# Kernel tuning notes

Hardware: AMD Instinct MI355X
Metric: run time of the kernel (lower is better)

The kernel has to match this reference:

```python
import jax, jax.numpy as jnp
import numpy as np

D_MODEL = 1024
N_HEADS = 16
HEAD_DIM = D_MODEL // N_HEADS


def setup_inputs() -> dict:
    key = jax.random.key(0)
    k1, k2, k3, k4, k5 = jax.random.split(key, 5)
    s = 1.0 / np.sqrt(D_MODEL)
    return {
        "x": jax.random.normal(k1, (2, 2048, D_MODEL), dtype=jnp.float32),
        "w_qkv": jax.random.normal(k2, (D_MODEL, 3 * D_MODEL), dtype=jnp.float32) * s,
        "b_qkv": jax.random.normal(k3, (3 * D_MODEL,), dtype=jnp.float32) * 0.02,
        "w_proj": jax.random.normal(k4, (D_MODEL, D_MODEL), dtype=jnp.float32) * s,
        "b_proj": jax.random.normal(k5, (D_MODEL,), dtype=jnp.float32) * 0.02,
    }


def reference(x, w_qkv, b_qkv, w_proj, b_proj):
    B, S, D = x.shape
    H, Hd = N_HEADS, HEAD_DIM
    qkv = x @ w_qkv + b_qkv                       # [B,S,3D]
    q, k, v = jnp.split(qkv, 3, axis=-1)
    # split heads -> [B,H,S,Hd]
    q = q.reshape(B, S, H, Hd).transpose(0, 2, 1, 3)
    k = k.reshape(B, S, H, Hd).transpose(0, 2, 1, 3)
    v = v.reshape(B, S, H, Hd).transpose(0, 2, 1, 3)
    scale = 1.0 / jnp.sqrt(jnp.asarray(Hd, dtype=x.dtype))
    scores = jnp.einsum("bhqd,bhkd->bhqk", q, k) * scale  # [B,H,S,S]
    causal = jnp.tril(jnp.ones((S, S), dtype=bool))
    scores = jnp.where(causal, scores, jnp.asarray(-jnp.inf, dtype=scores.dtype))
    attn = jax.nn.softmax(scores, axis=-1)
    out = jnp.einsum("bhqk,bhkd->bhqd", attn, v)  # [B,H,S,Hd]
    out = out.transpose(0, 2, 1, 3).reshape(B, S, D)
    return out @ w_proj + b_proj
```

## Files before the change

kernel.cpp:

```cpp
#include <hip/hip_runtime.h>


typedef float f32x4 __attribute__((ext_vector_type(4)));
typedef float f32x16 __attribute__((ext_vector_type(16)));
typedef short bf16x8 __attribute__((ext_vector_type(8)));

#if __has_builtin(__builtin_amdgcn_exp2f)
#define EXP2(x) __builtin_amdgcn_exp2f(x)
#else
#define EXP2(x) exp2f(x)
#endif

__device__ __forceinline__ unsigned short f2bf(float f) {
  union { float f; unsigned u; } v; v.f = f;
  unsigned u = v.u + 0x7fffu + ((v.u >> 16) & 1u);
  return (unsigned short)(u >> 16);
}

__device__ __forceinline__ void async_load16(const void* g, void* lds) {
  __builtin_amdgcn_global_load_lds(
      (const __attribute__((address_space(1))) void*)g,
      (__attribute__((address_space(3))) void*)lds, 16, 0, 0);
}

__global__ __launch_bounds__(256) void prep_kernel(
    const float* __restrict__ x, const float* __restrict__ w_qkv,
    const float* __restrict__ w_proj, unsigned short* __restrict__ Xb,
    unsigned short* __restrict__ WTq, unsigned short* __restrict__ WTp)
{
  const int bid = blockIdx.x;
  const int tid = threadIdx.x;
  if (bid < 4096) {
    const int i = (bid * 256 + tid) * 4;
    float4 f = *(const float4*)(x + i);
    ushort4 o;
    o.x = f2bf(f.x); o.y = f2bf(f.y); o.z = f2bf(f.z); o.w = f2bf(f.w);
    *(ushort4*)(Xb + i) = o;
  } else {
    __shared__ float tile[32][33];
    const float* in; unsigned short* out; int N, bx, by;
    if (bid < 7168) { const int b2 = bid - 4096; in = w_qkv;  out = WTq; N = 3072; bx = b2 % 96; by = b2 / 96; }
    else            { const int b3 = bid - 7168; in = w_proj; out = WTp; N = 1024; bx = b3 & 31; by = b3 >> 5; }
    const int tx = tid & 31, ty = tid >> 5;
    const int n0 = bx * 32, k0 = by * 32;
#pragma unroll
    for (int i = ty; i < 32; i += 8)
      tile[i][tx] = in[(size_t)(k0 + i) * N + (n0 + tx)];
    __syncthreads();
#pragma unroll
    for (int i = ty; i < 32; i += 8)
      out[(size_t)(n0 + i) * 1024 + (k0 + tx)] = f2bf(tile[tx][i]);
  }
}

template <int MI, int NI>
__device__ __forceinline__ void gemm_mainloop(
    const unsigned short* __restrict__ A,
    const unsigned short* __restrict__ BT,
    int K, int mBlk, int nBlk,
    unsigned short* As, unsigned short* Bs,
    f32x4 (&acc)[MI][NI], int lane, int wave)
{
  const int l16 = lane & 15, quad = lane >> 4;
  const int mW = (wave >> 1) * MI * 16;
  const int nW = (wave & 1) * NI * 16;
  constexpr int AROWS = 2 * MI * 16;
  constexpr int BROWS = 2 * NI * 16;
  constexpr int AINST = AROWS / 64;
  constexpr int BINST = BROWS / 64;
  const int rl = lane >> 2;
  const int cl = (lane & 3) * 8;

  for (int k0 = 0; k0 < K; k0 += 32) {
    __syncthreads();
#pragma unroll
    for (int t = 0; t < AINST; ++t) {
      const int rbase = wave * (AROWS / 4) + t * 16;
      async_load16(A + (size_t)(mBlk + rbase + rl) * K + k0 + cl, &As[rbase * 32]);
    }
#pragma unroll
    for (int t = 0; t < BINST; ++t) {
      const int rbase = wave * (BROWS / 4) + t * 16;
      async_load16(BT + (size_t)(nBlk + rbase + rl) * K + k0 + cl, &Bs[rbase * 32]);
    }
    __syncthreads();

    bf16x8 af[MI], bf[NI];
#pragma unroll
    for (int i = 0; i < MI; ++i)
      af[i] = *(const bf16x8*)&As[(mW + i * 16 + l16) * 32 + quad * 8];
#pragma unroll
    for (int j = 0; j < NI; ++j)
      bf[j] = *(const bf16x8*)&Bs[(nW + j * 16 + l16) * 32 + quad * 8];
#pragma unroll
    for (int i = 0; i < MI; ++i)
#pragma unroll
      for (int j = 0; j < NI; ++j)
        acc[i][j] = __builtin_amdgcn_mfma_f32_16x16x32_bf16(af[i], bf[j], acc[i][j], 0, 0, 0);
  }
}

__global__ __launch_bounds__(512, 2) void qkv_gemm_kernel(
    const unsigned short* __restrict__ A,
    const unsigned short* __restrict__ WT,
    const float* __restrict__ bias,
    unsigned short* __restrict__ QKV)
{
  __shared__ __align__(16) unsigned short Al[2][2][256][32];
  __shared__ __align__(16) unsigned short Bl[2][2][256][32];
  const int lane = threadIdx.x & 63;
  const int wave = threadIdx.x >> 6;
  const int l16 = lane & 15, quad = lane >> 4;
  const int wm = wave >> 2, wn = wave & 3;

  const int bid = blockIdx.x;
  const int xcd = bid & 7, rb = bid >> 3;
  const int bx = (xcd & 3) * 4 + (rb & 3);
  const int by = (xcd >> 2) * 6 + (rb >> 2);
  const int mBlk = bx * 256, nBlk = by * 256;

  const int srow = wave * 32 + (lane >> 2);
  const int scol = lane & 3;

  auto stage = [&](const unsigned short* __restrict__ G, int gRow0,
                   unsigned short (*L)[32], int kOff) {
#pragma unroll
    for (int i = 0; i < 2; ++i) {
      const int row = srow + i * 16;
      const int c = scol ^ ((row >> 1) & 3);
      async_load16(G + (size_t)(gRow0 + row) * 1024 + kOff + c * 8,
                   &L[wave * 32 + i * 16][0]);
    }
  };

  auto rdA = [&](int buf, int kh, int mi) -> bf16x8 {
    const int r = wm * 128 + mi * 16 + l16;
    return *(const bf16x8*)&Al[buf][kh][r][(quad ^ ((r >> 1) & 3)) * 8];
  };
  auto rdB = [&](int buf, int kh, int n) -> bf16x8 {
    const int r = wn * 64 + n * 16 + l16;
    return *(const bf16x8*)&Bl[buf][kh][r][(quad ^ ((r >> 1) & 3)) * 8];
  };

  f32x4 acc[8][4];
  const f32x4 z4 = {0.f, 0.f, 0.f, 0.f};
#pragma unroll
  for (int i = 0; i < 8; ++i)
#pragma unroll
    for (int j = 0; j < 4; ++j) acc[i][j] = z4;

  stage(A, mBlk, Al[0][0], 0);
  stage(WT, nBlk, Bl[0][0], 0);
  stage(A, mBlk, Al[0][1], 32);
  stage(WT, nBlk, Bl[0][1], 32);
  asm volatile("s_waitcnt vmcnt(4)\n\ts_barrier" ::: "memory");

  for (int t = 0; t < 16; ++t) {
    const int cur = t & 1, nxt = cur ^ 1;
    const int tn = (t + 1 < 16) ? t + 1 : 15;
    const int kO = tn * 64;
    bf16x8 bfr[4], afr[8];

    stage(A, mBlk, Al[nxt][0], kO);
    stage(WT, nBlk, Bl[nxt][0], kO);
#pragma unroll
    for (int n = 0; n < 4; ++n) bfr[n] = rdB(cur, 0, n);
#pragma unroll
    for (int i = 0; i < 8; ++i) afr[i] = rdA(cur, 0, i);
    __builtin_amdgcn_s_setprio(1);
#pragma unroll
    for (int i = 0; i < 8; ++i)
#pragma unroll
      for (int n = 0; n < 4; ++n)
        acc[i][n] = __builtin_amdgcn_mfma_f32_16x16x32_bf16(afr[i], bfr[n], acc[i][n], 0, 0, 0);
    __builtin_amdgcn_s_setprio(0);
    asm volatile("s_waitcnt vmcnt(4)\n\ts_barrier" ::: "memory");

    stage(A, mBlk, Al[nxt][1], kO + 32);
    stage(WT, nBlk, Bl[nxt][1], kO + 32);
#pragma unroll
    for (int n = 0; n < 4; ++n) bfr[n] = rdB(cur, 1, n);
#pragma unroll
    for (int i = 0; i < 8; ++i) afr[i] = rdA(cur, 1, i);
    __builtin_amdgcn_s_setprio(1);
#pragma unroll
    for (int i = 0; i < 8; ++i)
#pragma unroll
      for (int n = 0; n < 4; ++n)
        acc[i][n] = __builtin_amdgcn_mfma_f32_16x16x32_bf16(afr[i], bfr[n], acc[i][n], 0, 0, 0);
    __builtin_amdgcn_s_setprio(0);
    asm volatile("s_waitcnt vmcnt(4)\n\ts_barrier" ::: "memory");
  }
  asm volatile("s_waitcnt vmcnt(0)" ::: "memory");

  const int m0 = mBlk + wm * 128;
  const int n0 = nBlk + wn * 64;
  const int whichW = n0 >> 10;
  const int bb = m0 >> 11;
  const int sBase = (m0 & 2047);
  const size_t planeE = (size_t)2 * 16 * 2048 * 64;

  if (whichW == 2) {
    unsigned short* Vb = QKV + 2 * planeE;
#pragma unroll
    for (int j = 0; j < 4; ++j) {
      const int rem = (n0 & 1023) + j * 16 + l16;
      const int hh = rem >> 6, hd = rem & 63;
      const float bv = bias[n0 + j * 16 + l16];
      unsigned short* col = Vb + (((size_t)bb * 16 + hh) * 64 + hd) * 2048;
#pragma unroll
      for (int i = 0; i < 8; ++i) {
        unsigned short pk[4];
#pragma unroll
        for (int r = 0; r < 4; ++r) pk[r] = f2bf(acc[i][j][r] + bv);
        *(ushort4*)&col[sBase + i * 16 + quad * 4] = *(ushort4*)pk;
      }
    }
  } else {
    const float scale = (whichW == 0) ? 0.18033688011112042f : 1.0f;
#pragma unroll
    for (int j = 0; j < 4; ++j) {
      const int n = n0 + j * 16 + l16;
      const float bv = bias[n];
      const int rem = n & 1023;
      const int hh = rem >> 6, hd = rem & 63;
      unsigned short* pl = QKV + (size_t)whichW * planeE +
                           (((size_t)bb * 16 + hh) * 2048) * 64 + hd;
#pragma unroll
      for (int r = 0; r < 4; ++r) {
        const int s = sBase + (quad * 4 + r);
#pragma unroll
        for (int i = 0; i < 8; ++i)
          pl[(size_t)(s + i * 16) * 64] = f2bf((acc[i][j][r] + bv) * scale);
      }
    }
  }
}

__global__ __launch_bounds__(256, 2) void attn_kernel(
    const unsigned short* __restrict__ QKV,
    unsigned short* __restrict__ AO)
{
  __shared__ __align__(16) unsigned short Ks[3 * 64 * 64];
  __shared__ __align__(16) unsigned short Vs[3 * 64 * 64];
  const int lane = threadIdx.x & 63;
  const int wave = threadIdx.x >> 6;
  const int l31 = lane & 31;
  const int hi  = lane >> 5;

  const int lin  = blockIdx.x;
  const int xcd  = lin & 7;
  const int slot = lin >> 3;
  const int col  = xcd * 4 + (slot >> 4);
  const int b = col >> 4, h = col & 15;
  const int qg = (slot < 32) ? (slot & 15) : (15 - (slot & 15));
  const int qw = qg * 128 + wave * 32;

  const size_t planeE = (size_t)2 * 16 * 2048 * 64;
  const size_t bhS = ((size_t)b * 16 + h) * (size_t)(2048 * 64);
  const unsigned short* Q   = QKV + bhS;
  const unsigned short* Kg  = QKV + planeE + bhS;
  const unsigned short* VTg = QKV + 2 * planeE + bhS;

  bf16x8 qf_[4];
#pragma unroll
  for (int t = 0; t < 4; ++t)
    qf_[t] = *(const bf16x8*)(Q + (size_t)(qw + l31) * 64 + t * 16 + hi * 8);

  bf16x8 onesf;
#pragma unroll
  for (int i = 0; i < 8; ++i) onesf[i] = (short)0x3F80;

  f32x16 O[2], Osum;
#pragma unroll
  for (int r = 0; r < 16; ++r) { O[0][r] = 0.f; O[1][r] = 0.f; Osum[r] = 0.f; }

  const int tbase = (wave & 1) * 4;
  const bool doV = wave >= 2;

  auto stage = [&](int tileIdx, int bufIdx) {
    const int kt = tileIdx * 64;
    unsigned short* Kb = Ks + bufIdx * 4096;
    unsigned short* Vb = Vs + bufIdx * 4096;
#pragma unroll
    for (int i = 0; i < 4; ++i) {
      const int t = tbase + i;
      const int s = t * 64 + lane;
      const int row = s >> 3;
      const int c = (s & 7) ^ (row & 7);
      if (doV)
        async_load16(VTg + (size_t)row * 2048 + kt + c * 8, Vb + t * 512);
      else
        async_load16(Kg + (size_t)(kt + row) * 64 + c * 8, Kb + t * 512);
    }
  };

  const int nt = qg * 2 + 2;
  stage(0, 0);
  stage(1, 1);
  for (int ti = 0; ti < nt; ++ti) {
    asm volatile("s_waitcnt vmcnt(4)\n\ts_barrier" ::: "memory");
    const int tn = (ti + 2 < nt) ? ti + 2 : nt - 1;
    stage(tn, (ti + 2) % 3);
    const int kt = ti * 64;
    const unsigned short* Kb = Ks + (ti % 3) * 4096;
    const unsigned short* Vb = Vs + (ti % 3) * 4096;

    if (kt <= qw + 31) {
      const bool dmask = (kt + 63 > qw);
#pragma unroll
      for (int kg = 0; kg < 2; ++kg) {
        const int krow = kg * 32 + l31;
        const int ks7 = krow & 7;
        bf16x8 ka[4];
#pragma unroll
        for (int t = 0; t < 4; ++t)
          ka[t] = *(const bf16x8*)&Kb[(krow * 8 + ((t * 2 + hi) ^ ks7)) * 8];

        f32x16 sc;
#pragma unroll
        for (int r = 0; r < 16; ++r) sc[r] = 0.f;
        __builtin_amdgcn_s_setprio(1);
#pragma unroll
        for (int t = 0; t < 4; ++t)
          sc = __builtin_amdgcn_mfma_f32_32x32x16_bf16(ka[t], qf_[t], sc, 0, 0, 0);
        __builtin_amdgcn_s_setprio(0);

        float p[16];
#pragma unroll
        for (int r = 0; r < 16; ++r) {
          float v = sc[r];
          if (dmask) {
            const int key = kt + kg * 32 + (r & 3) + 8 * (r >> 2) + 4 * hi;
            if (key > qw + l31) v = -INFINITY;
          }
          p[r] = EXP2(v);
        }
        unsigned c8[8];
#pragma unroll
        for (int i = 0; i < 8; ++i)
          asm("v_cvt_pk_bf16_f32 %0, %1, %2"
              : "=v"(c8[i]) : "v"(p[2 * i]), "v"(p[2 * i + 1]));

#pragma unroll
        for (int half = 0; half < 2; ++half) {
          unsigned a0 = c8[4 * half + 0], a1 = c8[4 * half + 1];
          unsigned a2 = c8[4 * half + 2], a3 = c8[4 * half + 3];
          asm("v_permlane32_swap_b32 %0, %1" : "+v"(a0), "+v"(a2));
          asm("v_permlane32_swap_b32 %0, %1" : "+v"(a1), "+v"(a3));
          union { unsigned u[4]; bf16x8 v; } pa;
          pa.u[0] = a0; pa.u[1] = a1; pa.u[2] = a2; pa.u[3] = a3;
          const int kc = kg * 2 + half;

          __builtin_amdgcn_s_setprio(1);
          Osum = __builtin_amdgcn_mfma_f32_32x32x16_bf16(pa.v, onesf, Osum, 0, 0, 0);
#pragma unroll
          for (int g = 0; g < 2; ++g) {
            const int vrow = g * 32 + l31;
            bf16x8 vb = *(const bf16x8*)&Vb[(vrow * 8 + ((kc * 2 + hi) ^ (vrow & 7))) * 8];
            O[g] = __builtin_amdgcn_mfma_f32_32x32x16_bf16(pa.v, vb, O[g], 0, 0, 0);
          }
          __builtin_amdgcn_s_setprio(0);
        }
      }
    }
  }

  unsigned short* base = AO + ((size_t)b * 2048 + qw) * 1024 + h * 64 + l31;
#pragma unroll
  for (int r = 0; r < 16; ++r) {
    const float inv = 1.0f / Osum[r];
    const int row = (r & 3) + 8 * (r >> 2) + 4 * hi;
#pragma unroll
    for (int g = 0; g < 2; ++g)
      base[(size_t)row * 1024 + g * 32] = f2bf(O[g][r] * inv);
  }
}

__global__ __launch_bounds__(256) void proj_gemm_kernel(
    const unsigned short* __restrict__ A,
    const unsigned short* __restrict__ WT,
    const float* __restrict__ bias,
    float* __restrict__ out)
{
  __shared__ unsigned short As[64 * 32];
  __shared__ unsigned short Bs[128 * 32];
  const int lane = threadIdx.x & 63;
  const int wave = threadIdx.x >> 6;
  const int l16 = lane & 15, quad = lane >> 4;

  f32x4 acc[2][4];
  const f32x4 z4 = {0.f, 0.f, 0.f, 0.f};
#pragma unroll
  for (int i = 0; i < 2; ++i)
#pragma unroll
    for (int j = 0; j < 4; ++j) acc[i][j] = z4;

  gemm_mainloop<2, 4>(A, WT, 1024, blockIdx.x * 64, blockIdx.y * 128,
                      As, Bs, acc, lane, wave);

  const int m0 = blockIdx.x * 64 + (wave >> 1) * 32;
  const int n0 = blockIdx.y * 128 + (wave & 1) * 64;
#pragma unroll
  for (int i = 0; i < 2; ++i) {
#pragma unroll
    for (int j = 0; j < 4; ++j) {
      const int n = n0 + j * 16 + l16;
      const float bv = bias[n];
#pragma unroll
      for (int r = 0; r < 4; ++r) {
        const int m = m0 + i * 16 + quad * 4 + r;
        out[(size_t)m * 1024 + n] = acc[i][j][r] + bv;
      }
    }
  }
}

extern "C" void kernel_launch(void* const* d_in, const int* in_sizes, int n_in,
                              void* d_out, int out_size, void* d_ws, size_t ws_size,
                              hipStream_t stream) {
  const float* x      = (const float*)d_in[0];
  const float* w_qkv  = (const float*)d_in[1];
  const float* b_qkv  = (const float*)d_in[2];
  const float* w_proj = (const float*)d_in[3];
  const float* b_proj = (const float*)d_in[4];
  float* out = (float*)d_out;

  unsigned short* Xb  = (unsigned short*)d_ws;
  unsigned short* WTq = Xb + (size_t)4096 * 1024;
  unsigned short* WTp = WTq + (size_t)3072 * 1024;
  unsigned short* QKV = WTp + (size_t)1024 * 1024;
  unsigned short* AO  = QKV + (size_t)3 * 4096 * 1024;

  prep_kernel<<<8192, 256, 0, stream>>>(x, w_qkv, w_proj, Xb, WTq, WTp);
  qkv_gemm_kernel<<<192, 512, 0, stream>>>(Xb, WTq, b_qkv, QKV);
  attn_kernel<<<512, 256, 0, stream>>>(QKV, AO);
  proj_gemm_kernel<<<dim3(64, 8), 256, 0, stream>>>(AO, WTp, b_proj, out);
}
```

Before: 195.8 us.

## Fuse prep, QKV GEMM, attention and projection into one cooperative persistent kernel

Replaces the four separate launches with a single cooperative kernel of 256 blocks × 512 threads. The kernel runs each stage as a phase separated by grid-wide syncs and reuses one shared-memory buffer across phases. The attention phase pairs a short and a long causal query group in each block so work stays balanced. The projection phase is retiled to 128×128 blocks so it fits the fixed grid. The aim is to remove kernel launch gaps and tail effects, at the cost of grid.sync overhead and fewer, larger blocks for the memory-bound prep phase.

New measurement: 452.2 us. +130.9%, slower.

```diff
diff --git a/kernel.cpp b/kernel.cpp
--- a/kernel.cpp
+++ b/kernel.cpp
@@ -1,4 +1,7 @@
 #include <hip/hip_runtime.h>
+#include <hip/hip_cooperative_groups.h>
+
+namespace cg = cooperative_groups;
 
 
 typedef float f32x4 __attribute__((ext_vector_type(4)));
@@ -23,394 +26,370 @@
       (__attribute__((address_space(3))) void*)lds, 16, 0, 0);
 }
 
-__global__ __launch_bounds__(256) void prep_kernel(
+__global__ __launch_bounds__(512, 2) void fused_kernel(
     const float* __restrict__ x, const float* __restrict__ w_qkv,
-    const float* __restrict__ w_proj, unsigned short* __restrict__ Xb,
-    unsigned short* __restrict__ WTq, unsigned short* __restrict__ WTp)
+    const float* __restrict__ b_qkv, const float* __restrict__ w_proj,
+    const float* __restrict__ b_proj, float* __restrict__ out,
+    unsigned short* __restrict__ Xb, unsigned short* __restrict__ WTq,
+    unsigned short* __restrict__ WTp, unsigned short* __restrict__ QKV,
+    unsigned short* __restrict__ AO)
 {
+  __shared__ __align__(16) unsigned char smem[131072];
+  cg::grid_group grid = cg::this_grid();
   const int bid = blockIdx.x;
   const int tid = threadIdx.x;
-  if (bid < 4096) {
-    const int i = (bid * 256 + tid) * 4;
-    float4 f = *(const float4*)(x + i);
-    ushort4 o;
-    o.x = f2bf(f.x); o.y = f2bf(f.y); o.z = f2bf(f.z); o.w = f2bf(f.w);
-    *(ushort4*)(Xb + i) = o;
-  } else {
-    __shared__ float tile[32][33];
-    const float* in; unsigned short* out; int N, bx, by;
-    if (bid < 7168) { const int b2 = bid - 4096; in = w_qkv;  out = WTq; N = 3072; bx = b2 % 96; by = b2 / 96; }
-    else            { const int b3 = bid - 7168; in = w_proj; out = WTp; N = 1024; bx = b3 & 31; by = b3 >> 5; }
-    const int tx = tid & 31, ty = tid >> 5;
-    const int n0 = bx * 32, k0 = by * 32;
-#pragma unroll
-    for (int i = ty; i < 32; i += 8)
-      tile[i][tx] = in[(size_t)(k0 + i) * N + (n0 + tx)];
-    __syncthreads();
-#pragma unroll
-    for (int i = ty; i < 32; i += 8)
-      out[(size_t)(n0 + i) * 1024 + (k0 + tx)] = f2bf(tile[tx][i]);
+  const int lane = tid & 63;
+  const size_t planeE = (size_t)2 * 16 * 2048 * 64;
+
+  {
+    const int sub = tid >> 8, t256 = tid & 255;
+    float* tf = (float*)smem;
+#pragma unroll 1
+    for (int it = 0; it < 16; ++it) {
+      const int unit = bid * 32 + it * 2 + sub;
+      if (unit < 4096) {
+        const int i = (unit * 256 + t256) * 4;
+        float4 f = *(const float4*)(x + i);
+        ushort4 o;
+        o.x = f2bf(f.x); o.y = f2bf(f.y); o.z = f2bf(f.z); o.w = f2bf(f.w);
+        *(ushort4*)(Xb + i) = o;
+      } else {
+        const float* in; unsigned short* op; int N, bx2, by2;
+        if (unit < 7168) { const int b2 = unit - 4096; in = w_qkv;  op = WTq; N = 3072; bx2 = b2 % 96; by2 = b2 / 96; }
+        else             { const int b3 = unit - 7168; in = w_proj; op = WTp; N = 1024; bx2 = b3 & 31; by2 = b3 >> 5; }
+        const int tx = t256 & 31, ty = t256 >> 5;
+        const int n0 = bx2 * 32, k0 = by2 * 32;
+#pragma unroll
+        for (int i2 = ty; i2 < 32; i2 += 8)
+          tf[(sub * 32 + i2) * 33 + tx] = in[(size_t)(k0 + i2) * N + n0 + tx];
+        __syncthreads();
+#pragma unroll
+        for (int i2 = ty; i2 < 32; i2 += 8)
+          op[(size_t)(n0 + i2) * 1024 + k0 + tx] = f2bf(tf[(sub * 32 + tx) * 33 + i2]);
+        __syncthreads();
+      }
+    }
   }
-}
-
-template <int MI, int NI>
-__device__ __forceinline__ void gemm_mainloop(
-    const unsigned short* __restrict__ A,
-    const unsigned short* __restrict__ BT,
-    int K, int mBlk, int nBlk,
-    unsigned short* As, unsigned short* Bs,
-    f32x4 (&acc)[MI][NI], int lane, int wave)
-{
-  const int l16 = lane & 15, quad = lane >> 4;
-  const int mW = (wave >> 1) * MI * 16;
-  const int nW = (wave & 1) * NI * 16;
-  constexpr int AROWS = 2 * MI * 16;
-  constexpr int BROWS = 2 * NI * 16;
-  constexpr int AINST = AROWS / 64;
-  constexpr int BINST = BROWS / 64;
-  const int rl = lane >> 2;
-  const int cl = (lane & 3) * 8;
-
-  for (int k0 = 0; k0 < K; k0 += 32) {
-    __syncthreads();
-#pragma unroll
-    for (int t = 0; t < AINST; ++t) {
-      const int rbase = wave * (AROWS / 4) + t * 16;
-      async_load16(A + (size_t)(mBlk + rbase + rl) * K + k0 + cl, &As[rbase * 32]);
-    }
-#pragma unroll
-    for (int t = 0; t < BINST; ++t) {
-      const int rbase = wave * (BROWS / 4) + t * 16;
-      async_load16(BT + (size_t)(nBlk + rbase + rl) * K + k0 + cl, &Bs[rbase * 32]);
-    }
-    __syncthreads();
-
-    bf16x8 af[MI], bf[NI];
-#pragma unroll
-    for (int i = 0; i < MI; ++i)
-      af[i] = *(const bf16x8*)&As[(mW + i * 16 + l16) * 32 + quad * 8];
-#pragma unroll
-    for (int j = 0; j < NI; ++j)
-      bf[j] = *(const bf16x8*)&Bs[(nW + j * 16 + l16) * 32 + quad * 8];
-#pragma unroll
-    for (int i = 0; i < MI; ++i)
-#pragma unroll
-      for (int j = 0; j < NI; ++j)
-        acc[i][j] = __builtin_amdgcn_mfma_f32_16x16x32_bf16(af[i], bf[j], acc[i][j], 0, 0, 0);
+  __threadfence();
+  grid.sync();
+
+  if (bid < 192) {
+    unsigned short* AlB = (unsigned short*)smem;
+    unsigned short* BlB = AlB + 32768;
+    const int wave = tid >> 6;
+    const int l16 = lane & 15, quad = lane >> 4;
+    const int wm = wave >> 2, wn = wave & 3;
+    const int xcd = bid & 7, rb = bid >> 3;
+    const int bx = (xcd & 3) * 4 + (rb & 3);
+    const int by = (xcd >> 2) * 6 + (rb >> 2);
+    const int mBlk = bx * 256, nBlk = by * 256;
+    const int srow = wave * 32 + (lane >> 2);
+    const int scol = lane & 3;
+
+    auto stageQ = [&](const unsigned short* __restrict__ G, int gRow0,
+                      unsigned short* L, int kOff) {
+#pragma unroll
+      for (int i = 0; i < 2; ++i) {
+        const int row = srow + i * 16;
+        const int c = scol ^ ((row >> 1) & 3);
+        async_load16(G + (size_t)(gRow0 + row) * 1024 + kOff + c * 8,
+                     L + (wave * 32 + i * 16) * 32);
+      }
+    };
+    auto rdA = [&](int buf, int kh, int mi) -> bf16x8 {
+      const int r = wm * 128 + mi * 16 + l16;
+      return *(const bf16x8*)&AlB[(buf * 2 + kh) * 8192 + r * 32 + (quad ^ ((r >> 1) & 3)) * 8];
+    };
+    auto rdB = [&](int buf, int kh, int n) -> bf16x8 {
+      const int r = wn * 64 + n * 16 + l16;
+      return *(const bf16x8*)&BlB[(buf * 2 + kh) * 8192 + r * 32 + (quad ^ ((r >> 1) & 3)) * 8];
+    };
+
+    f32x4 acc[8][4];
+    const f32x4 z4 = {0.f, 0.f, 0.f, 0.f};
+#pragma unroll
+    for (int i = 0; i < 8; ++i)
+#pragma unroll
+      for (int j = 0; j < 4; ++j) acc[i][j] = z4;
+
+    stageQ(Xb, mBlk, AlB, 0);
+    stageQ(WTq, nBlk, BlB, 0);
+    stageQ(Xb, mBlk, AlB + 8192, 32);
+    stageQ(WTq, nBlk, BlB + 8192, 32);
+    asm volatile("s_waitcnt vmcnt(4)\n\ts_barrier" ::: "memory");
+
+    for (int t = 0; t < 16; ++t) {
+      const int cur = t & 1, nxt = cur ^ 1;
+      const int tn = (t + 1 < 16) ? t + 1 : 15;
+      const int kO = tn * 64;
+      bf16x8 bfr[4], afr[8];
+
+      stageQ(Xb, mBlk, AlB + (nxt * 2 + 0) * 8192, kO);
+      stageQ(WTq, nBlk, BlB + (nxt * 2 + 0) * 8192, kO);
+#pragma unroll
+      for (int n = 0; n < 4; ++n) bfr[n] = rdB(cur, 0, n);
+#pragma unroll
+      for (int i = 0; i < 8; ++i) afr[i] = rdA(cur, 0, i);
+      __builtin_amdgcn_s_setprio(1);
+#pragma unroll
+      for (int i = 0; i < 8; ++i)
+#pragma unroll
+        for (int n = 0; n < 4; ++n)
+          acc[i][n] = __builtin_amdgcn_mfma_f32_16x16x32_bf16(afr[i], bfr[n], acc[i][n], 0, 0, 0);
+      __builtin_amdgcn_s_setprio(0);
+      asm volatile("s_waitcnt vmcnt(4)\n\ts_barrier" ::: "memory");
+
+      stageQ(Xb, mBlk, AlB + (nxt * 2 + 1) * 8192, kO + 32);
+      stageQ(WTq, nBlk, BlB + (nxt * 2 + 1) * 8192, kO + 32);
+#pragma unroll
+      for (int n = 0; n < 4; ++n) bfr[n] = rdB(cur, 1, n);
+#pragma unroll
+      for (int i = 0; i < 8; ++i) afr[i] = rdA(cur, 1, i);
+      __builtin_amdgcn_s_setprio(1);
+#pragma unroll
+      for (int i = 0; i < 8; ++i)
+#pragma unroll
+        for (int n = 0; n < 4; ++n)
+          acc[i][n] = __builtin_amdgcn_mfma_f32_16x16x32_bf16(afr[i], bfr[n], acc[i][n], 0, 0, 0);
+      __builtin_amdgcn_s_setprio(0);
+      asm volatile("s_waitcnt vmcnt(4)\n\ts_barrier" ::: "memory");
+    }
+    asm volatile("s_waitcnt vmcnt(0)" ::: "memory");
+
+    const int m0 = mBlk + wm * 128;
+    const int n0 = nBlk + wn * 64;
+    const int whichW = n0 >> 10;
+    const int bb = m0 >> 11;
+    const int sBase = (m0 & 2047);
+
+    if (whichW == 2) {
+      unsigned short* Vb = QKV + 2 * planeE;
+#pragma unroll
+      for (int j = 0; j < 4; ++j) {
+        const int rem = (n0 & 1023) + j * 16 + l16;
+        const int hh = rem >> 6, hd = rem & 63;
+        const float bv = b_qkv[n0 + j * 16 + l16];
+        unsigned short* colp = Vb + (((size_t)bb * 16 + hh) * 64 + hd) * 2048;
+#pragma unroll
+        for (int i = 0; i < 8; ++i) {
+          unsigned short pk[4];
+#pragma unroll
+          for (int r = 0; r < 4; ++r) pk[r] = f2bf(acc[i][j][r] + bv);
+          *(ushort4*)&colp[sBase + i * 16 + quad * 4] = *(ushort4*)pk;
+        }
+      }
+    } else {
+      const float scale = (whichW == 0) ? 0.18033688011112042f : 1.0f;
+#pragma unroll
+      for (int j = 0; j < 4; ++j) {
+        const int n = n0 + j * 16 + l16;
+        const float bv = b_qkv[n];
+        const int rem = n & 1023;
+        const int hh = rem >> 6, hd = rem & 63;
+        unsigned short* pl = QKV + (size_t)whichW * planeE +
+                             (((size_t)bb * 16 + hh) * 2048) * 64 + hd;
+#pragma unroll
+        for (int r = 0; r < 4; ++r) {
+          const int s = sBase + (quad * 4 + r);
+#pragma unroll
+          for (int i = 0; i < 8; ++i)
+            pl[(size_t)(s + i * 16) * 64] = f2bf((acc[i][j][r] + bv) * scale);
+        }
+      }
+    }
   }
-}
-
-__global__ __launch_bounds__(512, 2) void qkv_gemm_kernel(
-    const unsigned short* __restrict__ A,
-    const unsigned short* __restrict__ WT,
-    const float* __restrict__ bias,
-    unsigned short* __restrict__ QKV)
-{
-  __shared__ __align__(16) unsigned short Al[2][2][256][32];
-  __shared__ __align__(16) unsigned short Bl[2][2][256][32];
-  const int lane = threadIdx.x & 63;
-  const int wave = threadIdx.x >> 6;
-  const int l16 = lane & 15, quad = lane >> 4;
-  const int wm = wave >> 2, wn = wave & 3;
-
-  const int bid = blockIdx.x;
-  const int xcd = bid & 7, rb = bid >> 3;
-  const int bx = (xcd & 3) * 4 + (rb & 3);
-  const int by = (xcd >> 2) * 6 + (rb >> 2);
-  const int mBlk = bx * 256, nBlk = by * 256;
-
-  const int srow = wave * 32 + (lane >> 2);
-  const int scol = lane & 3;
-
-  auto stage = [&](const unsigned short* __restrict__ G, int gRow0,
-                   unsigned short (*L)[32], int kOff) {
-#pragma unroll
-    for (int i = 0; i < 2; ++i) {
-      const int row = srow + i * 16;
-      const int c = scol ^ ((row >> 1) & 3);
-      async_load16(G + (size_t)(gRow0 + row) * 1024 + kOff + c * 8,
-                   &L[wave * 32 + i * 16][0]);
-    }
-  };
-
-  auto rdA = [&](int buf, int kh, int mi) -> bf16x8 {
-    const int r = wm * 128 + mi * 16 + l16;
-    return *(const bf16x8*)&Al[buf][kh][r][(quad ^ ((r >> 1) & 3)) * 8];
-  };
-  auto rdB = [&](int buf, int kh, int n) -> bf16x8 {
-    const int r = wn * 64 + n * 16 + l16;
-    return *(const bf16x8*)&Bl[buf][kh][r][(quad ^ ((r >> 1) & 3)) * 8];
-  };
-
-  f32x4 acc[8][4];
-  const f32x4 z4 = {0.f, 0.f, 0.f, 0.f};
-#pragma unroll
-  for (int i = 0; i < 8; ++i)
-#pragma unroll
-    for (int j = 0; j < 4; ++j) acc[i][j] = z4;
-
-  stage(A, mBlk, Al[0][0], 0);
-  stage(WT, nBlk, Bl[0][0], 0);
-  stage(A, mBlk, Al[0][1], 32);
-  stage(WT, nBlk, Bl[0][1], 32);
-  asm volatile("s_waitcnt vmcnt(4)\n\ts_barrier" ::: "memory");
-
-  for (int t = 0; t < 16; ++t) {
-    const int cur = t & 1, nxt = cur ^ 1;
-    const int tn = (t + 1 < 16) ? t + 1 : 15;
-    const int kO = tn * 64;
-    bf16x8 bfr[4], afr[8];
-
-    stage(A, mBlk, Al[nxt][0], kO);
-    stage(WT, nBlk, Bl[nxt][0], kO);
-#pragma unroll
-    for (int n = 0; n < 4; ++n) bfr[n] = rdB(cur, 0, n);
-#pragma unroll
-    for (int i = 0; i < 8; ++i) afr[i] = rdA(cur, 0, i);
-    __builtin_amdgcn_s_setprio(1);
-#pragma unroll
-    for (int i = 0; i < 8; ++i)
-#pragma unroll
-      for (int n = 0; n < 4; ++n)
-        acc[i][n] = __builtin_amdgcn_mfma_f32_16x16x32_bf16(afr[i], bfr[n], acc[i][n], 0, 0, 0);
-    __builtin_amdgcn_s_setprio(0);
-    asm volatile("s_waitcnt vmcnt(4)\n\ts_barrier" ::: "memory");
-
-    stage(A, mBlk, Al[nxt][1], kO + 32);
-    stage(WT, nBlk, Bl[nxt][1], kO + 32);
-#pragma unroll
-    for (int n = 0; n < 4; ++n) bfr[n] = rdB(cur, 1, n);
-#pragma unroll
-    for (int i = 0; i < 8; ++i) afr[i] = rdA(cur, 1, i);
-    __builtin_amdgcn_s_setprio(1);
-#pragma unroll
-    for (int i = 0; i < 8; ++i)
-#pragma unroll
-      for (int n = 0; n < 4; ++n)
-        acc[i][n] = __builtin_amdgcn_mfma_f32_16x16x32_bf16(afr[i], bfr[n], acc[i][n], 0, 0, 0);
-    __builtin_amdgcn_s_setprio(0);
-    asm volatile("s_waitcnt vmcnt(4)\n\ts_barrier" ::: "memory");
+  __threadfence();
+  grid.sync();
+
+  {
+    unsigned short* Ksu = (unsigned short*)smem;
+    unsigned short* Vsu = Ksu + 12288;
+    const int wave = tid >> 6;
+    const int sub = tid >> 8;
+    const int wave4 = wave & 3;
+    const int l31 = lane & 31, hi = lane >> 5;
+
+    const int xcd = bid & 7, w = bid >> 3;
+    const int col = xcd * 4 + (w >> 3);
+    const int b = col >> 4, h = col & 15;
+    const int p = w & 7;
+    const int qg = sub ? (15 - p) : p;
+    const int qw = qg * 128 + wave4 * 32;
+
+    const size_t bhS = ((size_t)b * 16 + h) * (size_t)(2048 * 64);
+    const unsigned short* Q   = QKV + bhS;
+    const unsigned short* Kg  = QKV + planeE + bhS;
+    const unsigned short* VTg = QKV + 2 * planeE + bhS;
+
+    bf16x8 qf_[4];
+#pragma unroll
+    for (int t = 0; t < 4; ++t)
+      qf_[t] = *(const bf16x8*)(Q + (size_t)(qw + l31) * 64 + t * 16 + hi * 8);
+
+    bf16x8 onesf;
+#pragma unroll
+    for (int i = 0; i < 8; ++i) onesf[i] = (short)0x3F80;
+
+    f32x16 O[2], Osum;
+#pragma unroll
+    for (int r = 0; r < 16; ++r) { O[0][r] = 0.f; O[1][r] = 0.f; Osum[r] = 0.f; }
+
+    const int tbase = (wave4 & 1) * 4;
+    const bool doV = (wave4 >= 2);
+    const bool doStage = (sub == 0);
+
+    auto stage = [&](int tileIdx, int bufIdx) {
+      if (!doStage) return;
+      const int kt = tileIdx * 64;
+      unsigned short* Kb = Ksu + bufIdx * 4096;
+      unsigned short* Vb = Vsu + bufIdx * 4096;
+#pragma unroll
+      for (int i = 0; i < 4; ++i) {
+        const int t = tbase + i;
+        const int s = t * 64 + lane;
+        const int row = s >> 3;
+        const int c = (s & 7) ^ (row & 7);
+        if (doV)
+          async_load16(VTg + (size_t)row * 2048 + kt + c * 8, Vb + t * 512);
+        else
+          async_load16(Kg + (size_t)(kt + row) * 64 + c * 8, Kb + t * 512);
+      }
+    };
+
+    stage(0, 0);
+    stage(1, 1);
+    for (int ti = 0; ti < 32; ++ti) {
+      asm volatile("s_waitcnt vmcnt(4)\n\ts_barrier" ::: "memory");
+      const int tn = (ti + 2 < 32) ? ti + 2 : 31;
+      stage(tn, (ti + 2) % 3);
+      const int kt = ti * 64;
+      const unsigned short* Kb = Ksu + (ti % 3) * 4096;
+      const unsigned short* Vb = Vsu + (ti % 3) * 4096;
+
+      if (kt <= qw + 31) {
+        const bool dmask = (kt + 63 > qw);
+#pragma unroll
+        for (int kg = 0; kg < 2; ++kg) {
+          const int krow = kg * 32 + l31;
+          const int ks7 = krow & 7;
+          bf16x8 ka[4];
+#pragma unroll
+          for (int t = 0; t < 4; ++t)
+            ka[t] = *(const bf16x8*)&Kb[(krow * 8 + ((t * 2 + hi) ^ ks7)) * 8];
+
+          f32x16 sc;
+#pragma unroll
+          for (int r = 0; r < 16; ++r) sc[r] = 0.f;
+          __builtin_amdgcn_s_setprio(1);
+#pragma unroll
+          for (int t = 0; t < 4; ++t)
+            sc = __builtin_amdgcn_mfma_f32_32x32x16_bf16(ka[t], qf_[t], sc, 0, 0, 0);
+          __builtin_amdgcn_s_setprio(0);
+
+          float pp[16];
+#pragma unroll
+          for (int r = 0; r < 16; ++r) {
+            float v = sc[r];
+            if (dmask) {
+              const int key = kt + kg * 32 + (r & 3) + 8 * (r >> 2) + 4 * hi;
+              if (key > qw + l31) v = -INFINITY;
+            }
+            pp[r] = EXP2(v);
+          }
+          unsigned c8[8];
+#pragma unroll
+          for (int i = 0; i < 8; ++i)
+            asm("v_cvt_pk_bf16_f32 %0, %1, %2"
+                : "=v"(c8[i]) : "v"(pp[2 * i]), "v"(pp[2 * i + 1]));
+
+#pragma unroll
+          for (int half = 0; half < 2; ++half) {
+            unsigned a0 = c8[4 * half + 0], a1 = c8[4 * half + 1];
+            unsigned a2 = c8[4 * half + 2], a3 = c8[4 * half + 3];
+            asm("v_permlane32_swap_b32 %0, %1" : "+v"(a0), "+v"(a2));
+            asm("v_permlane32_swap_b32 %0, %1" : "+v"(a1), "+v"(a3));
+            union { unsigned u[4]; bf16x8 v; } pa;
+            pa.u[0] = a0; pa.u[1] = a1; pa.u[2] = a2; pa.u[3] = a3;
+            const int kc = kg * 2 + half;
+
+            __builtin_amdgcn_s_setprio(1);
+            Osum = __builtin_amdgcn_mfma_f32_32x32x16_bf16(pa.v, onesf, Osum, 0, 0, 0);
+#pragma unroll
+            for (int g = 0; g < 2; ++g) {
+              const int vrow = g * 32 + l31;
+              bf16x8 vb = *(const bf16x8*)&Vb[(vrow * 8 + ((kc * 2 + hi) ^ (vrow & 7))) * 8];
+              O[g] = __builtin_amdgcn_mfma_f32_32x32x16_bf16(pa.v, vb, O[g], 0, 0, 0);
+            }
+            __builtin_amdgcn_s_setprio(0);
+          }
+        }
+      }
+    }
+    asm volatile("s_waitcnt vmcnt(0)" ::: "memory");
+
+    unsigned short* base = AO + ((size_t)b * 2048 + qw) * 1024 + h * 64 + l31;
+#pragma unroll
+    for (int r = 0; r < 16; ++r) {
+      const float inv = 1.0f / Osum[r];
+      const int row = (r & 3) + 8 * (r >> 2) + 4 * hi;
+#pragma unroll
+      for (int g = 0; g < 2; ++g)
+        base[(size_t)row * 1024 + g * 32] = f2bf(O[g][r] * inv);
+    }
   }
-  asm volatile("s_waitcnt vmcnt(0)" ::: "memory");
-
-  const int m0 = mBlk + wm * 128;
-  const int n0 = nBlk + wn * 64;
-  const int whichW = n0 >> 10;
-  const int bb = m0 >> 11;
-  const int sBase = (m0 & 2047);
-  const size_t planeE = (size_t)2 * 16 * 2048 * 64;
-
-  if (whichW == 2) {
-    unsigned short* Vb = QKV + 2 * planeE;
-#pragma unroll
-    for (int j = 0; j < 4; ++j) {
-      const int rem = (n0 & 1023) + j * 16 + l16;
-      const int hh = rem >> 6, hd = rem & 63;
-      const float bv = bias[n0 + j * 16 + l16];
-      unsigned short* col = Vb + (((size_t)bb * 16 + hh) * 64 + hd) * 2048;
-#pragma unroll
-      for (int i = 0; i < 8; ++i) {
-        unsigned short pk[4];
-#pragma unroll
-        for (int r = 0; r < 4; ++r) pk[r] = f2bf(acc[i][j][r] + bv);
-        *(ushort4*)&col[sBase + i * 16 + quad * 4] = *(ushort4*)pk;
-      }
-    }
-  } else {
-    const float scale = (whichW == 0) ? 0.18033688011112042f : 1.0f;
-#pragma unroll
-    for (int j = 0; j < 4; ++j) {
-      const int n = n0 + j * 16 + l16;
-      const float bv = bias[n];
-      const int rem = n & 1023;
-      const int hh = rem >> 6, hd = rem & 63;
-      unsigned short* pl = QKV + (size_t)whichW * planeE +
-                           (((size_t)bb * 16 + hh) * 2048) * 64 + hd;
-#pragma unroll
-      for (int r = 0; r < 4; ++r) {
-        const int s = sBase + (quad * 4 + r);
-#pragma unroll
-        for (int i = 0; i < 8; ++i)
-          pl[(size_t)(s + i * 16) * 64] = f2bf((acc[i][j][r] + bv) * scale);
-      }
-    }
-  }
-}
-
-__global__ __launch_bounds__(256, 2) void attn_kernel(
-    const unsigned short* __restrict__ QKV,
-    unsigned short* __restrict__ AO)
-{
-  __shared__ __align__(16) unsigned short Ks[3 * 64 * 64];
-  __shared__ __align__(16) unsigned short Vs[3 * 64 * 64];
-  const int lane = threadIdx.x & 63;
-  const int wave = threadIdx.x >> 6;
-  const int l31 = lane & 31;
-  const int hi  = lane >> 5;
-
-  const int lin  = blockIdx.x;
-  const int xcd  = lin & 7;
-  const int slot = lin >> 3;
-  const int col  = xcd * 4 + (slot >> 4);
-  const int b = col >> 4, h = col & 15;
-  const int qg = (slot < 32) ? (slot & 15) : (15 - (slot & 15));
-  const int qw = qg * 128 + wave * 32;
-
-  const size_t planeE = (size_t)2 * 16 * 2048 * 64;
-  const size_t bhS = ((size_t)b * 16 + h) * (size_t)(2048 * 64);
-  const unsigned short* Q   = QKV + bhS;
-  const unsigned short* Kg  = QKV + planeE + bhS;
-  const unsigned short* VTg = QKV + 2 * planeE + bhS;
-
-  bf16x8 qf_[4];
-#pragma unroll
-  for (int t = 0; t < 4; ++t)
-    qf_[t] = *(const bf16x8*)(Q + (size_t)(qw + l31) * 64 + t * 16 + hi * 8);
-
-  bf16x8 onesf;
-#pragma unroll
-  for (int i = 0; i < 8; ++i) onesf[i] = (short)0x3F80;
-
-  f32x16 O[2], Osum;
-#pragma unroll
-  for (int r = 0; r < 16; ++r) { O[0][r] = 0.f; O[1][r] = 0.f; Osum[r] = 0.f; }
-
-  const int tbase = (wave & 1) * 4;
-  const bool doV = wave >= 2;
-
-  auto stage = [&](int tileIdx, int bufIdx) {
-    const int kt = tileIdx * 64;
-    unsigned short* Kb = Ks + bufIdx * 4096;
-    unsigned short* Vb = Vs + bufIdx * 4096;
+  __threadfence();
+  grid.sync();
+
+  {
+    unsigned short* As = (unsigned short*)smem;
+    unsigned short* Bs = As + 4096;
+    const int wave = tid >> 6;
+    const int l16 = lane & 15, quad = lane >> 4;
+    const int wm = wave >> 2, wn = wave & 3;
+    const int nT = bid & 7, mT = bid >> 3;
+    const int mBlk = mT * 128, nBlk = nT * 128;
+    const int rl = lane >> 2, cl = (lane & 3) * 8;
+
+    f32x4 acc[4][2];
+    const f32x4 z4 = {0.f, 0.f, 0.f, 0.f};
+#pragma unroll
+    for (int i = 0; i < 4; ++i)
+#pragma unroll
+      for (int j = 0; j < 2; ++j) acc[i][j] = z4;
+
+    for (int k0 = 0; k0 < 1024; k0 += 32) {
+      __syncthreads();
+      async_load16(AO + (size_t)(mBlk + wave * 16 + rl) * 1024 + k0 + cl,
+                   As + (wave * 16) * 32);
+      async_load16(WTp + (size_t)(nBlk + wave * 16 + rl) * 1024 + k0 + cl,
+                   Bs + (wave * 16) * 32);
+      __syncthreads();
+
+      bf16x8 af[4], bf[2];
+#pragma unroll
+      for (int i = 0; i < 4; ++i)
+        af[i] = *(const bf16x8*)&As[(wm * 64 + i * 16 + l16) * 32 + quad * 8];
+#pragma unroll
+      for (int j = 0; j < 2; ++j)
+        bf[j] = *(const bf16x8*)&Bs[(wn * 32 + j * 16 + l16) * 32 + quad * 8];
+#pragma unroll
+      for (int i = 0; i < 4; ++i)
+#pragma unroll
+        for (int j = 0; j < 2; ++j)
+          acc[i][j] = __builtin_amdgcn_mfma_f32_16x16x32_bf16(af[i], bf[j], acc[i][j], 0, 0, 0);
+    }
+
 #pragma unroll
     for (int i = 0; i < 4; ++i) {
-      const int t = tbase + i;
-      const int s = t * 64 + lane;
-      const int row = s >> 3;
-      const int c = (s & 7) ^ (row & 7);
-      if (doV)
-        async_load16(VTg + (size_t)row * 2048 + kt + c * 8, Vb + t * 512);
-      else
-        async_load16(Kg + (size_t)(kt + row) * 64 + c * 8, Kb + t * 512);
-    }
-  };
-
-  const int nt = qg * 2 + 2;
-  stage(0, 0);
-  stage(1, 1);
-  for (int ti = 0; ti < nt; ++ti) {
-    asm volatile("s_waitcnt vmcnt(4)\n\ts_barrier" ::: "memory");
-    const int tn = (ti + 2 < nt) ? ti + 2 : nt - 1;
-    stage(tn, (ti + 2) % 3);
-    const int kt = ti * 64;
-    const unsigned short* Kb = Ks + (ti % 3) * 4096;
-    const unsigned short* Vb = Vs + (ti % 3) * 4096;
-
-    if (kt <= qw + 31) {
-      const bool dmask = (kt + 63 > qw);
-#pragma unroll
-      for (int kg = 0; kg < 2; ++kg) {
-        const int krow = kg * 32 + l31;
-        const int ks7 = krow & 7;
-        bf16x8 ka[4];
-#pragma unroll
-        for (int t = 0; t < 4; ++t)
-          ka[t] = *(const bf16x8*)&Kb[(krow * 8 + ((t * 2 + hi) ^ ks7)) * 8];
-
-        f32x16 sc;
-#pragma unroll
-        for (int r = 0; r < 16; ++r) sc[r] = 0.f;
-        __builtin_amdgcn_s_setprio(1);
-#pragma unroll
-        for (int t = 0; t < 4; ++t)
-          sc = __builtin_amdgcn_mfma_f32_32x32x16_bf16(ka[t], qf_[t], sc, 0, 0, 0);
-        __builtin_amdgcn_s_setprio(0);
-
-        float p[16];
-#pragma unroll
-        for (int r = 0; r < 16; ++r) {
-          float v = sc[r];
-          if (dmask) {
-            const int key = kt + kg * 32 + (r & 3) + 8 * (r >> 2) + 4 * hi;
-            if (key > qw + l31) v = -INFINITY;
-          }
-          p[r] = EXP2(v);
+#pragma unroll
+      for (int j = 0; j < 2; ++j) {
+        const int n = nBlk + wn * 32 + j * 16 + l16;
+        const float bv = b_proj[n];
+#pragma unroll
+        for (int r = 0; r < 4; ++r) {
+          const int m = mBlk + wm * 64 + i * 16 + quad * 4 + r;
+          out[(size_t)m * 1024 + n] = acc[i][j][r] + bv;
         }
-        unsigned c8[8];
-#pragma unroll
-        for (int i = 0; i < 8; ++i)
-          asm("v_cvt_pk_bf16_f32 %0, %1, %2"
-              : "=v"(c8[i]) : "v"(p[2 * i]), "v"(p[2 * i + 1]));
-
-#pragma unroll
-        for (int half = 0; half < 2; ++half) {
-          unsigned a0 = c8[4 * half + 0], a1 = c8[4 * half + 1];
-          unsigned a2 = c8[4 * half + 2], a3 = c8[4 * half + 3];
-          asm("v_permlane32_swap_b32 %0, %1" : "+v"(a0), "+v"(a2));
-          asm("v_permlane32_swap_b32 %0, %1" : "+v"(a1), "+v"(a3));
-          union { unsigned u[4]; bf16x8 v; } pa;
-          pa.u[0] = a0; pa.u[1] = a1; pa.u[2] = a2; pa.u[3] = a3;
-          const int kc = kg * 2 + half;
-
-          __builtin_amdgcn_s_setprio(1);
-          Osum = __builtin_amdgcn_mfma_f32_32x32x16_bf16(pa.v, onesf, Osum, 0, 0, 0);
-#pragma unroll
-          for (int g = 0; g < 2; ++g) {
-            const int vrow = g * 32 + l31;
-            bf16x8 vb = *(const bf16x8*)&Vb[(vrow * 8 + ((kc * 2 + hi) ^ (vrow & 7))) * 8];
-            O[g] = __builtin_amdgcn_mfma_f32_32x32x16_bf16(pa.v, vb, O[g], 0, 0, 0);
-          }
-          __builtin_amdgcn_s_setprio(0);
-        }
-      }
-    }
-  }
-
-  unsigned short* base = AO + ((size_t)b * 2048 + qw) * 1024 + h * 64 + l31;
-#pragma unroll
-  for (int r = 0; r < 16; ++r) {
-    const float inv = 1.0f / Osum[r];
-    const int row = (r & 3) + 8 * (r >> 2) + 4 * hi;
-#pragma unroll
-    for (int g = 0; g < 2; ++g)
-      base[(size_t)row * 1024 + g * 32] = f2bf(O[g][r] * inv);
-  }
-}
-
-__global__ __launch_bounds__(256) void proj_gemm_kernel(
-    const unsigned short* __restrict__ A,
-    const unsigned short* __restrict__ WT,
-    const float* __restrict__ bias,
-    float* __restrict__ out)
-{
-  __shared__ unsigned short As[64 * 32];
-  __shared__ unsigned short Bs[128 * 32];
-  const int lane = threadIdx.x & 63;
-  const int wave = threadIdx.x >> 6;
-  const int l16 = lane & 15, quad = lane >> 4;
-
-  f32x4 acc[2][4];
-  const f32x4 z4 = {0.f, 0.f, 0.f, 0.f};
-#pragma unroll
-  for (int i = 0; i < 2; ++i)
-#pragma unroll
-    for (int j = 0; j < 4; ++j) acc[i][j] = z4;
-
-  gemm_mainloop<2, 4>(A, WT, 1024, blockIdx.x * 64, blockIdx.y * 128,
-                      As, Bs, acc, lane, wave);
-
-  const int m0 = blockIdx.x * 64 + (wave >> 1) * 32;
-  const int n0 = blockIdx.y * 128 + (wave & 1) * 64;
-#pragma unroll
-  for (int i = 0; i < 2; ++i) {
-#pragma unroll
-    for (int j = 0; j < 4; ++j) {
-      const int n = n0 + j * 16 + l16;
-      const float bv = bias[n];
-#pragma unroll
-      for (int r = 0; r < 4; ++r) {
-        const int m = m0 + i * 16 + quad * 4 + r;
-        out[(size_t)m * 1024 + n] = acc[i][j][r] + bv;
       }
     }
   }
@@ -432,8 +411,8 @@
   unsigned short* QKV = WTp + (size_t)1024 * 1024;
   unsigned short* AO  = QKV + (size_t)3 * 4096 * 1024;
 
-  prep_kernel<<<8192, 256, 0, stream>>>(x, w_qkv, w_proj, Xb, WTq, WTp);
-  qkv_gemm_kernel<<<192, 512, 0, stream>>>(Xb, WTq, b_qkv, QKV);
-  attn_kernel<<<512, 256, 0, stream>>>(QKV, AO);
-  proj_gemm_kernel<<<dim3(64, 8), 256, 0, stream>>>(AO, WTp, b_proj, out);
+  void* args[] = {&x, &w_qkv, &b_qkv, &w_proj, &b_proj, &out,
+                  &Xb, &WTq, &WTp, &QKV, &AO};
+  hipLaunchCooperativeKernel((const void*)fused_kernel, dim3(256), dim3(512),
+                             args, 0, stream);
 }
```
